# Kernel tuning notes

Hardware: AMD Instinct MI355X
Metric: run time of the kernel (lower is better)

Reference implementation:

```python
import jax, jax.numpy as jnp
import numpy as np

N = 1024
D_IN = 512
D = 128
E = 8192


def setup_inputs() -> dict:
    key = jax.random.key(0)
    ks = jax.random.split(key, 7)
    return {
        "inputs": jax.random.normal(ks[0], (N, D_IN), dtype=jnp.float32),
        "adj": jax.random.uniform(ks[1], (N, N), dtype=jnp.float32),
        "weight": jax.random.normal(ks[2], (D_IN, D), dtype=jnp.float32) * 0.05,
        "weight_two": jax.random.normal(ks[3], (2 * D, D), dtype=jnp.float32) * 0.05,
        "weight_three": jax.random.normal(ks[4], (2 * D, 1), dtype=jnp.float32) * 0.05,
        "train_edges": jax.random.randint(ks[5], (E, 2), 0, N, dtype=jnp.int64 if jax.config.jax_enable_x64 else jnp.int32),
        "train_false_edges": jax.random.randint(ks[6], (E, 2), 0, N, dtype=jnp.int64 if jax.config.jax_enable_x64 else jnp.int32),
    }


def reference(inputs, adj, weight, weight_two, weight_three, train_edges, train_false_edges):
    # encoder: x = X W ; z = A x   (single GCN-style layer, no bias)
    x = inputs @ weight          # (N, D)
    z = adj @ x                  # (N, D)
    n, d = z.shape

    # all-pairs features: pair (i, j) -> [z_i ; z_j]  (torch repeat/reshape semantics)
    z1 = jnp.broadcast_to(z[:, None, :], (n, n, d))   # z1[i,j] = z[i]
    z2 = jnp.broadcast_to(z[None, :, :], (n, n, d))   # z2[i,j] = z[j]

    z_pair = jax.nn.relu(jnp.concatenate([z1, z2], axis=-1))   # (N, N, 2D)
    z_pair = jnp.einsum('ijk,kl->ijl', z_pair, weight_two)     # (N, N, D)
    z_em = z1 * z2                                             # (N, N, D)

    score = jnp.einsum('ijk,kl->ijl', jnp.concatenate([z_pair, z_em], axis=-1), weight_three)
    return jax.nn.sigmoid(score[..., 0])  # (N, N)
```

## Files before the change

### kernel.cpp

```cpp
#include <hip/hip_runtime.h>
#include <math.h>

#define NN 1024
#define DIN 512
#define DD 128

static constexpr long XP_OFF = 0;
static constexpr long ZP_OFF = XP_OFF + 4L * NN * DD;
static constexpr long X_OFF  = ZP_OFF + 8L * NN * DD;
static constexpr long Z_OFF  = X_OFF + (long)NN * DD;
static constexpr long U_OFF  = Z_OFF + (long)NN * DD;
static constexpr long A_OFF  = U_OFF + 256;
static constexpr long B_OFF  = A_OFF + NN;

__global__ __launch_bounds__(256) void gemm_part(
    const float* __restrict__ A, const float* __restrict__ B,
    float* __restrict__ Cp, int K, int Kc) {
  const int t = threadIdx.x;
  const int tx = t & 31;
  const int ty = t >> 5;
  const int row0 = blockIdx.x * 32;
  const int k0 = blockIdx.y * Kc;

  float acc[4][4] = {};

  for (int k = k0; k < k0 + Kc; k += 4) {
    float bv[4][4];
#pragma unroll
    for (int kk = 0; kk < 4; ++kk) {
      const float* Brow = &B[(long)(k + kk) * DD + tx];
#pragma unroll
      for (int mc = 0; mc < 4; ++mc) bv[kk][mc] = Brow[32 * mc];
    }
#pragma unroll
    for (int mr = 0; mr < 4; ++mr) {
      const int r = row0 + ty + 8 * mr;
      const float4 av = *(const float4*)&A[(long)r * K + k];
      const float ar[4] = {av.x, av.y, av.z, av.w};
#pragma unroll
      for (int kk = 0; kk < 4; ++kk)
#pragma unroll
        for (int mc = 0; mc < 4; ++mc) acc[mr][mc] += ar[kk] * bv[kk][mc];
    }
  }

  float* Cs = Cp + (long)blockIdx.y * NN * DD;
#pragma unroll
  for (int mr = 0; mr < 4; ++mr) {
    const int r = row0 + ty + 8 * mr;
#pragma unroll
    for (int mc = 0; mc < 4; ++mc) {
      Cs[(long)r * DD + tx + 32 * mc] = acc[mr][mc];
    }
  }
}

__global__ __launch_bounds__(256) void reduce_x_u(
    const float* __restrict__ xp, float* __restrict__ x,
    const float* __restrict__ W2, const float* __restrict__ w3,
    float* __restrict__ u) {
  const long i = (long)blockIdx.x * 256 + threadIdx.x;
  const long S = (long)NN * DD;
  x[i] = xp[i] + xp[S + i] + xp[2 * S + i] + xp[3 * S + i];

  if (blockIdx.x == 0) {
    const int kq = threadIdx.x;
    float uu = 0.f;
#pragma unroll 4
    for (int l = 0; l < DD; ++l) uu += W2[(long)kq * DD + l] * w3[l];
    u[kq] = uu;
  }
}

__global__ __launch_bounds__(64) void finalize_z(
    const float* __restrict__ zp, float* __restrict__ z,
    const float* __restrict__ u, const float* __restrict__ w3,
    float* __restrict__ a, float* __restrict__ b) {
  const int i = blockIdx.x;
  const int t = threadIdx.x;
  const long S = (long)NN * DD;
  float acc_a = 0.f, acc_b = 0.f;
#pragma unroll
  for (int m = 0; m < 2; ++m) {
    const int k = t + 64 * m;
    float s = 0.f;
#pragma unroll
    for (int p = 0; p < 8; ++p) s += zp[p * S + (long)i * DD + k];
    z[(long)i * DD + k] = s;
    const float rz = s > 0.f ? s : 0.f;
    acc_a += rz * u[k];
    acc_b += rz * u[DD + k];
  }
#pragma unroll
  for (int off = 32; off > 0; off >>= 1) {
    acc_a += __shfl_down(acc_a, off);
    acc_b += __shfl_down(acc_b, off);
  }
  if (t == 0) {
    a[i] = acc_a;
    b[i] = acc_b;
  }
}

__global__ __launch_bounds__(256) void decode_tile(
    const float* __restrict__ z, const float* __restrict__ w3,
    const float* __restrict__ a, const float* __restrict__ b,
    float* __restrict__ out) {
  __shared__ float zl[64 * DD];
  __shared__ float zwl[64 * DD];
  const int t = threadIdx.x;
  const int i0 = blockIdx.y * 64;
  const int j0 = blockIdx.x * 64;

#pragma unroll
  for (int s = 0; s < 8; ++s) {
    const int q = s * 256 + t;
    const int r = q >> 5;
    const int k4 = (q & 31) << 2;
    const int sw = r * DD + (k4 ^ ((r & 7) << 2));
    const float4 v = *(const float4*)&z[(long)(i0 + r) * DD + k4];
    *(float4*)&zl[sw] = v;
    float4 w = *(const float4*)&z[(long)(j0 + r) * DD + k4];
    const float4 c = *(const float4*)&w3[DD + k4];
    w.x *= c.x; w.y *= c.y; w.z *= c.z; w.w *= c.w;
    *(float4*)&zwl[sw] = w;
  }
  __syncthreads();

  const int tx = t & 15;
  const int ty = t >> 4;
  float acc[4][4] = {};

  for (int k4 = 0; k4 < DD; k4 += 4) {
    float4 ar[4], bc[4];
#pragma unroll
    for (int m = 0; m < 4; ++m) {
      const int R = ty + 16 * m;
      ar[m] = *(const float4*)&zl[R * DD + (k4 ^ ((R & 7) << 2))];
    }
#pragma unroll
    for (int m = 0; m < 4; ++m) {
      const int C = tx + 16 * m;
      bc[m] = *(const float4*)&zwl[C * DD + (k4 ^ ((C & 7) << 2))];
    }
#pragma unroll
    for (int mr = 0; mr < 4; ++mr)
#pragma unroll
      for (int mc = 0; mc < 4; ++mc)
        acc[mr][mc] += ar[mr].x * bc[mc].x + ar[mr].y * bc[mc].y +
                       ar[mr].z * bc[mc].z + ar[mr].w * bc[mc].w;
  }

#pragma unroll
  for (int mr = 0; mr < 4; ++mr) {
    const int i = i0 + ty + 16 * mr;
    const float ai = a[i];
#pragma unroll
    for (int mc = 0; mc < 4; ++mc) {
      const int j = j0 + tx + 16 * mc;
      const float s = ai + b[j] + acc[mr][mc];
      out[(long)i * NN + j] = 1.0f / (1.0f + __expf(-s));
    }
  }
}

extern "C" void kernel_launch(void* const* d_in, const int* in_sizes, int n_in,
                              void* d_out, int out_size, void* d_ws, size_t ws_size,
                              hipStream_t stream) {
  (void)in_sizes; (void)n_in; (void)out_size; (void)ws_size;
  const float* inputs = (const float*)d_in[0];
  const float* adj    = (const float*)d_in[1];
  const float* weight = (const float*)d_in[2];
  const float* W2     = (const float*)d_in[3];
  const float* w3     = (const float*)d_in[4];
  float* out = (float*)d_out;

  float* ws = (float*)d_ws;
  float* xp = ws + XP_OFF;
  float* zp = ws + ZP_OFF;
  float* x  = ws + X_OFF;
  float* z  = ws + Z_OFF;
  float* u  = ws + U_OFF;
  float* a  = ws + A_OFF;
  float* b  = ws + B_OFF;

  gemm_part<<<dim3(32, 4), 256, 0, stream>>>(inputs, weight, xp, DIN, DIN / 4);
  reduce_x_u<<<512, 256, 0, stream>>>(xp, x, W2, w3, u);
  gemm_part<<<dim3(32, 8), 256, 0, stream>>>(adj, x, zp, NN, NN / 8);
  finalize_z<<<1024, 64, 0, stream>>>(zp, z, u, w3, a, b);
  decode_tile<<<dim3(16, 16), 256, 0, stream>>>(z, w3, a, b, out);
}
```

Measured before the change: 115.3 us.

## Fuse encoder GEMMs and decoder into one cooperative kernel with grid syncs

```diff
diff --git a/kernel.cpp b/kernel.cpp
--- a/kernel.cpp
+++ b/kernel.cpp
@@ -1,165 +1,171 @@
 #include <hip/hip_runtime.h>
+#include <hip/hip_cooperative_groups.h>
 #include <math.h>
+
+namespace cg = cooperative_groups;
 
 #define NN 1024
 #define DIN 512
 #define DD 128
 
-static constexpr long XP_OFF = 0;
-static constexpr long ZP_OFF = XP_OFF + 4L * NN * DD;
-static constexpr long X_OFF  = ZP_OFF + 8L * NN * DD;
-static constexpr long Z_OFF  = X_OFF + (long)NN * DD;
-static constexpr long U_OFF  = Z_OFF + (long)NN * DD;
-static constexpr long A_OFF  = U_OFF + 256;
-static constexpr long B_OFF  = A_OFF + NN;
+static constexpr long X_OFF = 0;
+static constexpr long Z_OFF = X_OFF + (long)NN * DD;
+static constexpr long U_OFF = Z_OFF + (long)NN * DD;
+static constexpr long A_OFF = U_OFF + 256;
+static constexpr long B_OFF = A_OFF + NN;
 
-__global__ __launch_bounds__(256) void gemm_part(
-    const float* __restrict__ A, const float* __restrict__ B,
-    float* __restrict__ Cp, int K, int Kc) {
+__global__ __launch_bounds__(256) void fused_encdec(
+    const float* __restrict__ inputs, const float* __restrict__ adj,
+    const float* __restrict__ W, const float* __restrict__ W2,
+    const float* __restrict__ w3, float* __restrict__ out,
+    float* __restrict__ x, float* __restrict__ z, float* __restrict__ u,
+    float* __restrict__ a, float* __restrict__ b) {
+  __shared__ float lds[16384];
+  cg::grid_group grid = cg::this_grid();
   const int t = threadIdx.x;
-  const int tx = t & 31;
-  const int ty = t >> 5;
-  const int row0 = blockIdx.x * 32;
-  const int k0 = blockIdx.y * Kc;
+  const int blk = blockIdx.x;
 
-  float acc[4][4] = {};
+  {
+    const float* src = inputs + (long)blk * 4 * DIN;
+#pragma unroll
+    for (int j = 0; j < 2; ++j) {
+      const int e = t * 8 + j * 4;
+      *(float4*)&lds[e] = *(const float4*)&src[e];
+    }
+    __syncthreads();
+    const int kh = t >> 7;
+    const int r  = (t >> 5) & 3;
+    const int c4 = (t & 31) * 4;
+    float a0 = 0.f, a1 = 0.f, a2 = 0.f, a3 = 0.f;
+    const int k0 = kh * (DIN / 2);
+#pragma unroll 4
+    for (int k = k0; k < k0 + DIN / 2; ++k) {
+      const float4 w = *(const float4*)&W[(long)k * DD + c4];
+      const float av = lds[r * DIN + k];
+      a0 += av * w.x; a1 += av * w.y; a2 += av * w.z; a3 += av * w.w;
+    }
+    float4 p; p.x = a0; p.y = a1; p.z = a2; p.w = a3;
+    *(float4*)&lds[8192 + (kh * 4 + r) * DD + c4] = p;
+    __syncthreads();
+    if (kh == 0) {
+      const float4 p0 = *(const float4*)&lds[8192 + r * DD + c4];
+      const float4 p1 = *(const float4*)&lds[8192 + 512 + r * DD + c4];
+      float4 v;
+      v.x = p0.x + p1.x; v.y = p0.y + p1.y;
+      v.z = p0.z + p1.z; v.w = p0.w + p1.w;
+      *(float4*)&x[(long)(blk * 4 + r) * DD + c4] = v;
+    }
+    if (blk < 8 && t < 32) {
+      const int row = blk * 32 + t;
+      float s = 0.f;
+#pragma unroll 4
+      for (int l = 0; l < DD; ++l) s += W2[(long)row * DD + l] * w3[l];
+      u[row] = s;
+    }
+  }
+  grid.sync();
 
-  for (int k = k0; k < k0 + Kc; k += 4) {
-    float bv[4][4];
+  {
+    const float* src = adj + (long)blk * 4 * NN;
 #pragma unroll
-    for (int kk = 0; kk < 4; ++kk) {
-      const float* Brow = &B[(long)(k + kk) * DD + tx];
+    for (int j = 0; j < 4; ++j) {
+      const int e = t * 16 + j * 4;
+      *(float4*)&lds[e] = *(const float4*)&src[e];
+    }
+    __syncthreads();
+    const int kh = t >> 7;
+    const int r  = (t >> 5) & 3;
+    const int c4 = (t & 31) * 4;
+    float a0 = 0.f, a1 = 0.f, a2 = 0.f, a3 = 0.f;
+    const int k0 = kh * (NN / 2);
+#pragma unroll 4
+    for (int k = k0; k < k0 + NN / 2; ++k) {
+      const float4 xv = *(const float4*)&x[(long)k * DD + c4];
+      const float av = lds[r * NN + k];
+      a0 += av * xv.x; a1 += av * xv.y; a2 += av * xv.z; a3 += av * xv.w;
+    }
+    float4 p; p.x = a0; p.y = a1; p.z = a2; p.w = a3;
+    *(float4*)&lds[8192 + (kh * 4 + r) * DD + c4] = p;
+    __syncthreads();
+    if (kh == 0) {
+      const float4 p0 = *(const float4*)&lds[8192 + r * DD + c4];
+      const float4 p1 = *(const float4*)&lds[8192 + 512 + r * DD + c4];
+      float4 v;
+      v.x = p0.x + p1.x; v.y = p0.y + p1.y;
+      v.z = p0.z + p1.z; v.w = p0.w + p1.w;
+      *(float4*)&z[(long)(blk * 4 + r) * DD + c4] = v;
+      const float4 u0 = *(const float4*)&u[c4];
+      const float4 u1 = *(const float4*)&u[DD + c4];
+      const float rx = v.x > 0.f ? v.x : 0.f;
+      const float ry = v.y > 0.f ? v.y : 0.f;
+      const float rz = v.z > 0.f ? v.z : 0.f;
+      const float rw = v.w > 0.f ? v.w : 0.f;
+      float pa = rx * u0.x + ry * u0.y + rz * u0.z + rw * u0.w;
+      float pb = rx * u1.x + ry * u1.y + rz * u1.z + rw * u1.w;
 #pragma unroll
-      for (int mc = 0; mc < 4; ++mc) bv[kk][mc] = Brow[32 * mc];
+      for (int off = 16; off > 0; off >>= 1) {
+        pa += __shfl_down(pa, off, 32);
+        pb += __shfl_down(pb, off, 32);
+      }
+      if ((t & 31) == 0) {
+        a[blk * 4 + r] = pa;
+        b[blk * 4 + r] = pb;
+      }
+    }
+  }
+  grid.sync();
+
+  {
+    float* zl  = lds;
+    float* zwl = lds + 8192;
+    const int i0 = (blk >> 4) * 64;
+    const int j0 = (blk & 15) * 64;
+#pragma unroll
+    for (int s = 0; s < 8; ++s) {
+      const int q = s * 256 + t;
+      const int r = q >> 5;
+      const int k4 = (q & 31) << 2;
+      const int sw = r * DD + (k4 ^ ((r & 7) << 2));
+      *(float4*)&zl[sw] = *(const float4*)&z[(long)(i0 + r) * DD + k4];
+      float4 w = *(const float4*)&z[(long)(j0 + r) * DD + k4];
+      const float4 c = *(const float4*)&w3[DD + k4];
+      w.x *= c.x; w.y *= c.y; w.z *= c.z; w.w *= c.w;
+      *(float4*)&zwl[sw] = w;
+    }
+    __syncthreads();
+
+    const int tx = t & 15;
+    const int ty = t >> 4;
+    float acc[4][4] = {};
+    for (int k4 = 0; k4 < DD; k4 += 4) {
+      float4 ar[4], bc[4];
+#pragma unroll
+      for (int m = 0; m < 4; ++m) {
+        const int R = ty + 16 * m;
+        ar[m] = *(const float4*)&zl[R * DD + (k4 ^ ((R & 7) << 2))];
+      }
+#pragma unroll
+      for (int m = 0; m < 4; ++m) {
+        const int C = tx + 16 * m;
+        bc[m] = *(const float4*)&zwl[C * DD + (k4 ^ ((C & 7) << 2))];
+      }
+#pragma unroll
+      for (int mr = 0; mr < 4; ++mr)
+#pragma unroll
+        for (int mc = 0; mc < 4; ++mc)
+          acc[mr][mc] += ar[mr].x * bc[mc].x + ar[mr].y * bc[mc].y +
+                         ar[mr].z * bc[mc].z + ar[mr].w * bc[mc].w;
     }
 #pragma unroll
     for (int mr = 0; mr < 4; ++mr) {
-      const int r = row0 + ty + 8 * mr;
-      const float4 av = *(const float4*)&A[(long)r * K + k];
-      const float ar[4] = {av.x, av.y, av.z, av.w};
+      const int i = i0 + ty + 16 * mr;
+      const float ai = a[i];
 #pragma unroll
-      for (int kk = 0; kk < 4; ++kk)
-#pragma unroll
-        for (int mc = 0; mc < 4; ++mc) acc[mr][mc] += ar[kk] * bv[kk][mc];
-    }
-  }
-
-  float* Cs = Cp + (long)blockIdx.y * NN * DD;
-#pragma unroll
-  for (int mr = 0; mr < 4; ++mr) {
-    const int r = row0 + ty + 8 * mr;
-#pragma unroll
-    for (int mc = 0; mc < 4; ++mc) {
-      Cs[(long)r * DD + tx + 32 * mc] = acc[mr][mc];
-    }
-  }
-}
-
-__global__ __launch_bounds__(256) void reduce_x_u(
-    const float* __restrict__ xp, float* __restrict__ x,
-    const float* __restrict__ W2, const float* __restrict__ w3,
-    float* __restrict__ u) {
-  const long i = (long)blockIdx.x * 256 + threadIdx.x;
-  const long S = (long)NN * DD;
-  x[i] = xp[i] + xp[S + i] + xp[2 * S + i] + xp[3 * S + i];
-
-  if (blockIdx.x == 0) {
-    const int kq = threadIdx.x;
-    float uu = 0.f;
-#pragma unroll 4
-    for (int l = 0; l < DD; ++l) uu += W2[(long)kq * DD + l] * w3[l];
-    u[kq] = uu;
-  }
-}
-
-__global__ __launch_bounds__(64) void finalize_z(
-    const float* __restrict__ zp, float* __restrict__ z,
-    const float* __restrict__ u, const float* __restrict__ w3,
-    float* __restrict__ a, float* __restrict__ b) {
-  const int i = blockIdx.x;
-  const int t = threadIdx.x;
-  const long S = (long)NN * DD;
-  float acc_a = 0.f, acc_b = 0.f;
-#pragma unroll
-  for (int m = 0; m < 2; ++m) {
-    const int k = t + 64 * m;
-    float s = 0.f;
-#pragma unroll
-    for (int p = 0; p < 8; ++p) s += zp[p * S + (long)i * DD + k];
-    z[(long)i * DD + k] = s;
-    const float rz = s > 0.f ? s : 0.f;
-    acc_a += rz * u[k];
-    acc_b += rz * u[DD + k];
-  }
-#pragma unroll
-  for (int off = 32; off > 0; off >>= 1) {
-    acc_a += __shfl_down(acc_a, off);
-    acc_b += __shfl_down(acc_b, off);
-  }
-  if (t == 0) {
-    a[i] = acc_a;
-    b[i] = acc_b;
-  }
-}
-
-__global__ __launch_bounds__(256) void decode_tile(
-    const float* __restrict__ z, const float* __restrict__ w3,
-    const float* __restrict__ a, const float* __restrict__ b,
-    float* __restrict__ out) {
-  __shared__ float zl[64 * DD];
-  __shared__ float zwl[64 * DD];
-  const int t = threadIdx.x;
-  const int i0 = blockIdx.y * 64;
-  const int j0 = blockIdx.x * 64;
-
-#pragma unroll
-  for (int s = 0; s < 8; ++s) {
-    const int q = s * 256 + t;
-    const int r = q >> 5;
-    const int k4 = (q & 31) << 2;
-    const int sw = r * DD + (k4 ^ ((r & 7) << 2));
-    const float4 v = *(const float4*)&z[(long)(i0 + r) * DD + k4];
-    *(float4*)&zl[sw] = v;
-    float4 w = *(const float4*)&z[(long)(j0 + r) * DD + k4];
-    const float4 c = *(const float4*)&w3[DD + k4];
-    w.x *= c.x; w.y *= c.y; w.z *= c.z; w.w *= c.w;
-    *(float4*)&zwl[sw] = w;
-  }
-  __syncthreads();
-
-  const int tx = t & 15;
-  const int ty = t >> 4;
-  float acc[4][4] = {};
-
-  for (int k4 = 0; k4 < DD; k4 += 4) {
-    float4 ar[4], bc[4];
-#pragma unroll
-    for (int m = 0; m < 4; ++m) {
-      const int R = ty + 16 * m;
-      ar[m] = *(const float4*)&zl[R * DD + (k4 ^ ((R & 7) << 2))];
-    }
-#pragma unroll
-    for (int m = 0; m < 4; ++m) {
-      const int C = tx + 16 * m;
-      bc[m] = *(const float4*)&zwl[C * DD + (k4 ^ ((C & 7) << 2))];
-    }
-#pragma unroll
-    for (int mr = 0; mr < 4; ++mr)
-#pragma unroll
-      for (int mc = 0; mc < 4; ++mc)
-        acc[mr][mc] += ar[mr].x * bc[mc].x + ar[mr].y * bc[mc].y +
-                       ar[mr].z * bc[mc].z + ar[mr].w * bc[mc].w;
-  }
-
-#pragma unroll
-  for (int mr = 0; mr < 4; ++mr) {
-    const int i = i0 + ty + 16 * mr;
-    const float ai = a[i];
-#pragma unroll
-    for (int mc = 0; mc < 4; ++mc) {
-      const int j = j0 + tx + 16 * mc;
-      const float s = ai + b[j] + acc[mr][mc];
-      out[(long)i * NN + j] = 1.0f / (1.0f + __expf(-s));
+      for (int mc = 0; mc < 4; ++mc) {
+        const int j = j0 + tx + 16 * mc;
+        const float s = ai + b[j] + acc[mr][mc];
+        out[(long)i * NN + j] = 1.0f / (1.0f + __expf(-s));
+      }
     }
   }
 }
@@ -176,17 +182,15 @@
   float* out = (float*)d_out;
 
   float* ws = (float*)d_ws;
-  float* xp = ws + XP_OFF;
-  float* zp = ws + ZP_OFF;
-  float* x  = ws + X_OFF;
-  float* z  = ws + Z_OFF;
-  float* u  = ws + U_OFF;
-  float* a  = ws + A_OFF;
-  float* b  = ws + B_OFF;
+  float* x = ws + X_OFF;
+  float* z = ws + Z_OFF;
+  float* u = ws + U_OFF;
+  float* a = ws + A_OFF;
+  float* b = ws + B_OFF;
 
-  gemm_part<<<dim3(32, 4), 256, 0, stream>>>(inputs, weight, xp, DIN, DIN / 4);
-  reduce_x_u<<<512, 256, 0, stream>>>(xp, x, W2, w3, u);
-  gemm_part<<<dim3(32, 8), 256, 0, stream>>>(adj, x, zp, NN, NN / 8);
-  finalize_z<<<1024, 64, 0, stream>>>(zp, z, u, w3, a, b);
-  decode_tile<<<dim3(16, 16), 256, 0, stream>>>(z, w3, a, b, out);
+  void* args[] = {(void*)&inputs, (void*)&adj, (void*)&weight, (void*)&W2,
+                  (void*)&w3, (void*)&out, (void*)&x, (void*)&z, (void*)&u,
+                  (void*)&a, (void*)&b};
+  hipLaunchCooperativeKernel((const void*)fused_encdec, dim3(256), dim3(256),
+                             args, 0, stream);
 }
```

New measurement: 195.2 us. +69.3%, slower.

## Fuse split-K GEMMs with reductions into two row-block kernels

Applied to the files above, without the earlier changes.

```diff
diff --git a/kernel.cpp b/kernel.cpp
--- a/kernel.cpp
+++ b/kernel.cpp
@@ -5,100 +5,85 @@
 #define DIN 512
 #define DD 128
 
-static constexpr long XP_OFF = 0;
-static constexpr long ZP_OFF = XP_OFF + 4L * NN * DD;
-static constexpr long X_OFF  = ZP_OFF + 8L * NN * DD;
-static constexpr long Z_OFF  = X_OFF + (long)NN * DD;
-static constexpr long U_OFF  = Z_OFF + (long)NN * DD;
-static constexpr long A_OFF  = U_OFF + 256;
-static constexpr long B_OFF  = A_OFF + NN;
+static constexpr long X_OFF = 0;
+static constexpr long Z_OFF = X_OFF + (long)NN * DD;
+static constexpr long U_OFF = Z_OFF + (long)NN * DD;
+static constexpr long A_OFF = U_OFF + 256;
+static constexpr long B_OFF = A_OFF + NN;
 
-__global__ __launch_bounds__(256) void gemm_part(
-    const float* __restrict__ A, const float* __restrict__ B,
-    float* __restrict__ Cp, int K, int Kc) {
+__global__ __launch_bounds__(1024, 4) void k1_x_u(
+    const float* __restrict__ inputs, const float* __restrict__ W,
+    const float* __restrict__ W2, const float* __restrict__ w3,
+    float* __restrict__ x, float* __restrict__ u) {
+  __shared__ float arow[8 * DIN];
   const int t = threadIdx.x;
-  const int tx = t & 31;
-  const int ty = t >> 5;
-  const int row0 = blockIdx.x * 32;
-  const int k0 = blockIdx.y * Kc;
+  const int blk = blockIdx.x;
 
-  float acc[4][4] = {};
+  ((float4*)arow)[t] = ((const float4*)(inputs + (long)blk * 8 * DIN))[t];
+  __syncthreads();
 
-  for (int k = k0; k < k0 + Kc; k += 4) {
-    float bv[4][4];
+  const int c = t & 127;
+  const int rh = t >> 7;
+  const float* wp = W + c;
+  const float* ap = arow + rh * DIN;
+  float acc = 0.f;
+#pragma unroll 16
+  for (int k = 0; k < DIN; ++k) acc += ap[k] * wp[(long)k * DD];
+  x[(long)(blk * 8 + rh) * DD + c] = acc;
+
+  if (blk < 8 && t < 256) {
+    const int row = blk * 32 + (t >> 3);
+    const int l8 = t & 7;
+    float s = 0.f;
 #pragma unroll
-    for (int kk = 0; kk < 4; ++kk) {
-      const float* Brow = &B[(long)(k + kk) * DD + tx];
-#pragma unroll
-      for (int mc = 0; mc < 4; ++mc) bv[kk][mc] = Brow[32 * mc];
+    for (int i = 0; i < 16; ++i) {
+      const int l = l8 + 8 * i;
+      s += W2[(long)row * DD + l] * w3[l];
     }
 #pragma unroll
-    for (int mr = 0; mr < 4; ++mr) {
-      const int r = row0 + ty + 8 * mr;
-      const float4 av = *(const float4*)&A[(long)r * K + k];
-      const float ar[4] = {av.x, av.y, av.z, av.w};
-#pragma unroll
-      for (int kk = 0; kk < 4; ++kk)
-#pragma unroll
-        for (int mc = 0; mc < 4; ++mc) acc[mr][mc] += ar[kk] * bv[kk][mc];
-    }
-  }
-
-  float* Cs = Cp + (long)blockIdx.y * NN * DD;
-#pragma unroll
-  for (int mr = 0; mr < 4; ++mr) {
-    const int r = row0 + ty + 8 * mr;
-#pragma unroll
-    for (int mc = 0; mc < 4; ++mc) {
-      Cs[(long)r * DD + tx + 32 * mc] = acc[mr][mc];
-    }
+    for (int off = 4; off > 0; off >>= 1) s += __shfl_down(s, off, 8);
+    if (l8 == 0) u[row] = s;
   }
 }
 
-__global__ __launch_bounds__(256) void reduce_x_u(
-    const float* __restrict__ xp, float* __restrict__ x,
-    const float* __restrict__ W2, const float* __restrict__ w3,
-    float* __restrict__ u) {
-  const long i = (long)blockIdx.x * 256 + threadIdx.x;
-  const long S = (long)NN * DD;
-  x[i] = xp[i] + xp[S + i] + xp[2 * S + i] + xp[3 * S + i];
+__global__ __launch_bounds__(1024, 4) void k2_z_ab(
+    const float* __restrict__ adj, const float* __restrict__ x,
+    const float* __restrict__ u, float* __restrict__ z,
+    float* __restrict__ a, float* __restrict__ b) {
+  __shared__ float arow[8 * NN];
+  __shared__ float red[16][2];
+  const int t = threadIdx.x;
+  const int blk = blockIdx.x;
 
-  if (blockIdx.x == 0) {
-    const int kq = threadIdx.x;
-    float uu = 0.f;
-#pragma unroll 4
-    for (int l = 0; l < DD; ++l) uu += W2[(long)kq * DD + l] * w3[l];
-    u[kq] = uu;
-  }
-}
+  const float4* src = (const float4*)(adj + (long)blk * 8 * NN);
+#pragma unroll
+  for (int s = 0; s < 2; ++s) ((float4*)arow)[s * 1024 + t] = src[s * 1024 + t];
+  __syncthreads();
 
-__global__ __launch_bounds__(64) void finalize_z(
-    const float* __restrict__ zp, float* __restrict__ z,
-    const float* __restrict__ u, const float* __restrict__ w3,
-    float* __restrict__ a, float* __restrict__ b) {
-  const int i = blockIdx.x;
-  const int t = threadIdx.x;
-  const long S = (long)NN * DD;
-  float acc_a = 0.f, acc_b = 0.f;
-#pragma unroll
-  for (int m = 0; m < 2; ++m) {
-    const int k = t + 64 * m;
-    float s = 0.f;
-#pragma unroll
-    for (int p = 0; p < 8; ++p) s += zp[p * S + (long)i * DD + k];
-    z[(long)i * DD + k] = s;
-    const float rz = s > 0.f ? s : 0.f;
-    acc_a += rz * u[k];
-    acc_b += rz * u[DD + k];
-  }
+  const int c = t & 127;
+  const int rh = t >> 7;
+  const float* xp = x + c;
+  const float* ap = arow + rh * NN;
+  float acc = 0.f;
+#pragma unroll 16
+  for (int k = 0; k < NN; ++k) acc += ap[k] * xp[(long)k * DD];
+  const int row = blk * 8 + rh;
+  z[(long)row * DD + c] = acc;
+
+  const float r = acc > 0.f ? acc : 0.f;
+  float pa = r * u[c];
+  float pb = r * u[DD + c];
 #pragma unroll
   for (int off = 32; off > 0; off >>= 1) {
-    acc_a += __shfl_down(acc_a, off);
-    acc_b += __shfl_down(acc_b, off);
+    pa += __shfl_down(pa, off);
+    pb += __shfl_down(pb, off);
   }
-  if (t == 0) {
-    a[i] = acc_a;
-    b[i] = acc_b;
+  const int w = t >> 6;
+  if ((t & 63) == 0) { red[w][0] = pa; red[w][1] = pb; }
+  __syncthreads();
+  if (t < 8) {
+    a[blk * 8 + t] = red[2 * t][0] + red[2 * t + 1][0];
+    b[blk * 8 + t] = red[2 * t][1] + red[2 * t + 1][1];
   }
 }
 
@@ -118,8 +103,7 @@
     const int r = q >> 5;
     const int k4 = (q & 31) << 2;
     const int sw = r * DD + (k4 ^ ((r & 7) << 2));
-    const float4 v = *(const float4*)&z[(long)(i0 + r) * DD + k4];
-    *(float4*)&zl[sw] = v;
+    *(float4*)&zl[sw] = *(const float4*)&z[(long)(i0 + r) * DD + k4];
     float4 w = *(const float4*)&z[(long)(j0 + r) * DD + k4];
     const float4 c = *(const float4*)&w3[DD + k4];
     w.x *= c.x; w.y *= c.y; w.z *= c.z; w.w *= c.w;
@@ -130,7 +114,6 @@
   const int tx = t & 15;
   const int ty = t >> 4;
   float acc[4][4] = {};
-
   for (int k4 = 0; k4 < DD; k4 += 4) {
     float4 ar[4], bc[4];
 #pragma unroll
@@ -176,17 +159,13 @@
   float* out = (float*)d_out;
 
   float* ws = (float*)d_ws;
-  float* xp = ws + XP_OFF;
-  float* zp = ws + ZP_OFF;
-  float* x  = ws + X_OFF;
-  float* z  = ws + Z_OFF;
-  float* u  = ws + U_OFF;
-  float* a  = ws + A_OFF;
-  float* b  = ws + B_OFF;
+  float* x = ws + X_OFF;
+  float* z = ws + Z_OFF;
+  float* u = ws + U_OFF;
+  float* a = ws + A_OFF;
+  float* b = ws + B_OFF;
 
-  gemm_part<<<dim3(32, 4), 256, 0, stream>>>(inputs, weight, xp, DIN, DIN / 4);
-  reduce_x_u<<<512, 256, 0, stream>>>(xp, x, W2, w3, u);
-  gemm_part<<<dim3(32, 8), 256, 0, stream>>>(adj, x, zp, NN, NN / 8);
-  finalize_z<<<1024, 64, 0, stream>>>(zp, z, u, w3, a, b);
+  k1_x_u<<<128, 1024, 0, stream>>>(inputs, weight, W2, w3, x, u);
+  k2_z_ab<<<128, 1024, 0, stream>>>(adj, x, u, z, a, b);
   decode_tile<<<dim3(16, 16), 256, 0, stream>>>(z, w3, a, b, out);
 }
```

After: 126.5 us. 9.7% more time.
